# Performance work log

Measured on AMD Instinct MI355X. Metric: run time of the kernel, lower is better.

## Reference

```python
import jax, jax.numpy as jnp
import numpy as np

C = 512
NH = 8
GROUPS = 32
EPS = 1e-5


def setup_inputs() -> dict:
    key = jax.random.key(0)
    ks = jax.random.split(key, 7)
    B, T, H, W = 4, 24, 32, 32
    x = jax.random.normal(ks[0], (B, C, T, H, W), dtype=jnp.float32)
    gn_w = jnp.ones((C,), jnp.float32)
    gn_b = jnp.zeros((C,), jnp.float32)
    # 1x1 Conv1d weights stored as [out_ch, in_ch] (kernel dim of size 1 dropped)
    qkv_w = jax.random.normal(ks[1], (3 * C, C), dtype=jnp.float32) / np.sqrt(C)
    qkv_b = jax.random.normal(ks[2], (3 * C,), dtype=jnp.float32) * 0.02
    proj_w = jax.random.normal(ks[3], (C, C), dtype=jnp.float32) / np.sqrt(C)
    proj_b = jax.random.normal(ks[4], (C,), dtype=jnp.float32) * 0.02
    return {"x": x, "gn_w": gn_w, "gn_b": gn_b, "qkv_w": qkv_w,
            "qkv_b": qkv_b, "proj_w": proj_w, "proj_b": proj_b}


def reference(x, gn_w, gn_b, qkv_w, qkv_b, proj_w, proj_b):
    B, Cc, T, H, W = x.shape
    hd = Cc // NH
    # [B,C,T,H,W] -> [B*H*W, C, T]
    xf = jnp.transpose(x, (0, 3, 4, 1, 2)).reshape(B * H * W, Cc, T)
    # GroupNorm over (C/G, T) per group
    xg = xf.reshape(-1, GROUPS, Cc // GROUPS, T)
    mean = xg.mean(axis=(2, 3), keepdims=True)
    var = xg.var(axis=(2, 3), keepdims=True)
    xn = ((xg - mean) * jax.lax.rsqrt(var + EPS)).reshape(-1, Cc, T)
    xn = xn * gn_w[:, None] + gn_b[:, None]
    # 1x1 conv QKV: [n, 3C, T]
    qkv = jnp.einsum('nct,dc->ndt', xn, qkv_w) + qkv_b[:, None]
    qkv = qkv.reshape(-1, 3, NH, hd, T)
    q, k, v = qkv[:, 0], qkv[:, 1], qkv[:, 2]  # each [n, h, d, T]
    scale = 1.0 / np.sqrt(hd)
    attn = jax.nn.softmax(jnp.einsum('nhdt,nhds->nhts', q, k) * scale, axis=-1)
    out = jnp.einsum('nhts,nhds->nhtd', attn, v)        # [n, h, T, d]
    out = out.transpose(0, 2, 1, 3).reshape(-1, T, Cc)   # [n, T, C]
    out = out.transpose(0, 2, 1)                         # [n, C, T]
    out = jnp.einsum('nct,dc->ndt', out, proj_w) + proj_b[:, None]
    out = out.reshape(B, H, W, Cc, T).transpose(0, 3, 4, 1, 2)
    return x + out
```

## Files before the change

kernel.cpp:

```cpp
#include <hip/hip_runtime.h>
#include <hip/hip_bf16.h>
#include <stdint.h>

#define C_    512
#define T_    24
#define HWSZ  1024
#define NN    4096
#define JTOT  98304
#define EPSV  1e-5f

typedef short short8 __attribute__((ext_vector_type(8)));
typedef short short4v __attribute__((ext_vector_type(4)));
typedef float f32x4 __attribute__((ext_vector_type(4)));
typedef float f32x2 __attribute__((ext_vector_type(2)));
typedef __bf16 bf16x2 __attribute__((ext_vector_type(2)));

typedef __attribute__((address_space(1))) const uint32_t glob_u32;
typedef __attribute__((address_space(3))) uint32_t lds_u32;

#if __has_builtin(__builtin_amdgcn_fdot2_f32_bf16)
#define HAS_DOT2 1
#else
#define HAS_DOT2 0
#endif

__device__ __forceinline__ unsigned short f2bf(float f) {
  union { float f; unsigned u; } v; v.f = f;
  unsigned r = v.u + 0x7fffu + ((v.u >> 16) & 1u);
  return (unsigned short)(r >> 16);
}
__device__ __forceinline__ float bf2f(unsigned short b) {
  union { unsigned u; float f; } v; v.u = ((unsigned)b) << 16;
  return v.f;
}
__device__ __forceinline__ float bflo(uint32_t u) {
  union { unsigned u; float f; } v; v.u = u << 16; return v.f;
}
__device__ __forceinline__ float bfhi(uint32_t u) {
  union { unsigned u; float f; } v; v.u = u & 0xffff0000u; return v.f;
}
__device__ __forceinline__ uint32_t pkbf(float a, float b) {
  return (uint32_t)f2bf(a) | ((uint32_t)f2bf(b) << 16);
}
__device__ __forceinline__ bf16x2 asbf2(uint32_t u) {
  union { uint32_t u; bf16x2 v; } c; c.u = u; return c.v;
}

__device__ __forceinline__ void gload_lds16(const void* g, void* l) {
  __builtin_amdgcn_global_load_lds((glob_u32*)g, (lds_u32*)l, 16, 0, 0);
}

__global__ void k_cvt(const float* __restrict__ qkvw, const float* __restrict__ projw,
                      unsigned short* __restrict__ qkvw_bf, unsigned short* __restrict__ projw_bf) {
  int i = blockIdx.x * 256 + threadIdx.x;
  if (i < 786432) qkvw_bf[i] = f2bf(qkvw[i]);
  if (i < 262144) projw_bf[i] = f2bf(projw[i]);
}

__global__ __launch_bounds__(256) void k_stats(const float* __restrict__ x,
                                               float* __restrict__ mean, float* __restrict__ rstd) {
  int bid = blockIdx.x;
  int g = bid & 31, hwt = (bid >> 5) & 15, b = bid >> 9;
  int tid = threadIdx.x, lane = tid & 63, grp = tid >> 6;
  int hw = hwt * 64 + lane;
  float s = 0.f, sq = 0.f;
  for (int ct = grp; ct < 384; ct += 4) {
    int c = g * 16 + ct / 24;
    int t = ct % 24;
    float v = x[((size_t)((b * 512 + c) * 24 + t) << 10) + hw];
    s += v; sq += v * v;
  }
  __shared__ float ls[4][64], lq[4][64];
  ls[grp][lane] = s; lq[grp][lane] = sq;
  __syncthreads();
  if (tid < 64) {
    float S = ls[0][tid] + ls[1][tid] + ls[2][tid] + ls[3][tid];
    float Q = lq[0][tid] + lq[1][tid] + lq[2][tid] + lq[3][tid];
    float m = S * (1.f / 384.f);
    float var = Q * (1.f / 384.f) - m * m;
    int n = b * HWSZ + hwt * 64 + tid;
    mean[n * 32 + g] = m;
    rstd[n * 32 + g] = rsqrtf(var + EPSV);
  }
}

__global__ __launch_bounds__(256) void k_norm(const float* __restrict__ x,
                                              const float* __restrict__ mean, const float* __restrict__ rstd,
                                              const float* __restrict__ gnw, const float* __restrict__ gnb,
                                              unsigned short* __restrict__ xn) {
  __shared__ unsigned short xs[64][260];
  const int bid = blockIdx.x;
  const int hwt = bid & 15;
  const int chalf = (bid >> 4) & 1;
  const int tb = bid >> 5;
  const int t = tb % 24, b = tb / 24;
  const int hw0 = hwt * 64;
  const int tid = threadIdx.x;
  const int w = tid >> 6, lane = tid & 63;

  const int cslot = w * 4 + (lane >> 4);
  const int hwr = (lane & 15) * 4;
#pragma unroll
  for (int k = 0; k < 8; ++k) {
    const int crel = k * 32 + cslot * 2;
    const int c = chalf * 256 + crel;
    const float4 v0 = *reinterpret_cast<const float4*>(
        &x[(((size_t)(b * 512 + c) * 24 + t) << 10) + hw0 + hwr]);
    const float4 v1 = *reinterpret_cast<const float4*>(
        &x[(((size_t)(b * 512 + c + 1) * 24 + t) << 10) + hw0 + hwr]);
    *reinterpret_cast<uint32_t*>(&xs[hwr + 0][crel]) = pkbf(v0.x, v1.x);
    *reinterpret_cast<uint32_t*>(&xs[hwr + 1][crel]) = pkbf(v0.y, v1.y);
    *reinterpret_cast<uint32_t*>(&xs[hwr + 2][crel]) = pkbf(v0.z, v1.z);
    *reinterpret_cast<uint32_t*>(&xs[hwr + 3][crel]) = pkbf(v0.w, v1.w);
  }

  const int crel8 = (lane & 31) * 8;
  const int c8 = chalf * 256 + crel8;
  const int g = c8 >> 4;
  float gw[8], gb[8];
#pragma unroll
  for (int i = 0; i < 8; ++i) { gw[i] = gnw[c8 + i]; gb[i] = gnb[c8 + i]; }
  float mm[8], rr[8];
#pragma unroll
  for (int p = 0; p < 8; ++p) {
    const int nrel = (p * 4 + w) * 2 + (lane >> 5);
    const int ng = b * HWSZ + hw0 + nrel;
    mm[p] = mean[ng * 32 + g];
    rr[p] = rstd[ng * 32 + g];
  }
  __syncthreads();

#pragma unroll
  for (int p = 0; p < 8; ++p) {
    const int nrel = (p * 4 + w) * 2 + (lane >> 5);
    const short4v lo = *reinterpret_cast<const short4v*>(&xs[nrel][crel8]);
    const short4v hi = *reinterpret_cast<const short4v*>(&xs[nrel][crel8 + 4]);
    float y[8];
#pragma unroll
    for (int i = 0; i < 4; ++i) {
      y[i]     = (bf2f((unsigned short)lo[i]) - mm[p]) * rr[p] * gw[i]     + gb[i];
      y[i + 4] = (bf2f((unsigned short)hi[i]) - mm[p]) * rr[p] * gw[i + 4] + gb[i + 4];
    }
    uint4 wv;
    wv.x = pkbf(y[0], y[1]);
    wv.y = pkbf(y[2], y[3]);
    wv.z = pkbf(y[4], y[5]);
    wv.w = pkbf(y[6], y[7]);
    const size_t j = (size_t)t * NN + b * HWSZ + hw0 + nrel;
    *reinterpret_cast<uint4*>(&xn[j * C_ + c8]) = wv;
  }
}

#define STAGE8(mat, half, tile, Gptr, row0)                                           \
  {                                                                                   \
    unsigned short* _l = &lds[(((tile) & 1) * 2 + (mat))][half][(w * 2) * 512];       \
    const unsigned short* _g = (Gptr) +                                               \
        (size_t)((row0) + (half) * 128 + (w * 2) * 8 + srow) * 512 +                  \
        (tile) * 64 + sslot * 8;                                                      \
    gload_lds16(_g, _l);                                                              \
    gload_lds16(_g + 8 * 512, _l + 512);                                              \
  }

__global__ __launch_bounds__(512, 2) void k_gemm8(
    const unsigned short* __restrict__ A,
    const unsigned short* __restrict__ B,
    const float* __restrict__ bias,
    unsigned short* __restrict__ outb) {
  __shared__ __attribute__((aligned(16))) unsigned short lds[4][2][8192];
  const int bid = blockIdx.x;
  const int cpx = 2304 >> 3;
  const int lid = (bid & 7) * cpx + (bid >> 3);
  const int mt = lid % 6, jt = lid / 6;
  const int m0 = mt * 256, j0 = jt * 256;
  const int tid = threadIdx.x;
  const int w = tid >> 6, lane = tid & 63;
  const int l16 = lane & 15, lqq = lane >> 4;
  const int wm = w >> 2, wn = w & 3;
  const int srow = lane >> 3;
  const int sslot = (lane & 7) ^ srow;
  const int k0off = l16 * 64 + ((lqq ^ (l16 & 7)) * 8);
  const int k1off = l16 * 64 + (((lqq + 4) ^ (l16 & 7)) * 8);

  f32x4 acc[8][4];
#pragma unroll
  for (int i = 0; i < 8; ++i)
#pragma unroll
    for (int j = 0; j < 4; ++j) acc[i][j] = {0.f, 0.f, 0.f, 0.f};

  STAGE8(0, 0, 0, A, m0); STAGE8(0, 1, 0, A, m0);
  STAGE8(1, 0, 0, B, j0); STAGE8(1, 1, 0, B, j0);
  STAGE8(0, 0, 1, A, m0); STAGE8(0, 1, 1, A, m0);
  STAGE8(1, 0, 1, B, j0);
  asm volatile("s_waitcnt vmcnt(6)" ::: "memory");
  __builtin_amdgcn_s_barrier();

  for (int t = 0; t < 8; ++t) {
    const int buf = t & 1;
    const unsigned short* Ab = &lds[buf * 2 + 0][wm][0];
    const unsigned short* Bb = &lds[buf * 2 + 1][wn >> 1][(wn & 1) * 4096];
    short8 a[8][2], bb[4][2];
#pragma unroll
    for (int rr = 0; rr < 8; ++rr) {
      a[rr][0] = *reinterpret_cast<const short8*>(Ab + rr * 1024 + k0off);
      a[rr][1] = *reinterpret_cast<const short8*>(Ab + rr * 1024 + k1off);
    }
#pragma unroll
    for (int cc = 0; cc < 2; ++cc) {
      bb[cc][0] = *reinterpret_cast<const short8*>(Bb + cc * 1024 + k0off);
      bb[cc][1] = *reinterpret_cast<const short8*>(Bb + cc * 1024 + k1off);
    }
    if (t < 7) STAGE8(1, 1, t + 1, B, j0);
    asm volatile("" ::: "memory");
    __builtin_amdgcn_s_barrier();
    asm volatile("s_waitcnt lgkmcnt(0)" ::: "memory");
    __builtin_amdgcn_sched_barrier(0);
    __builtin_amdgcn_s_setprio(1);
#pragma unroll
    for (int rr = 0; rr < 4; ++rr)
#pragma unroll
      for (int cc = 0; cc < 2; ++cc) {
        acc[rr][cc] = __builtin_amdgcn_mfma_f32_16x16x32_bf16(a[rr][0], bb[cc][0], acc[rr][cc], 0, 0, 0);
        acc[rr][cc] = __builtin_amdgcn_mfma_f32_16x16x32_bf16(a[rr][1], bb[cc][1], acc[rr][cc], 0, 0, 0);
      }
    __builtin_amdgcn_s_setprio(0);
    asm volatile("" ::: "memory");
    __builtin_amdgcn_s_barrier();
#pragma unroll
    for (int cc = 2; cc < 4; ++cc) {
      bb[cc][0] = *reinterpret_cast<const short8*>(Bb + cc * 1024 + k0off);
      bb[cc][1] = *reinterpret_cast<const short8*>(Bb + cc * 1024 + k1off);
    }
    if (t < 6) STAGE8(0, 0, t + 2, A, m0);
    asm volatile("" ::: "memory");
    __builtin_amdgcn_s_barrier();
    asm volatile("s_waitcnt lgkmcnt(0)" ::: "memory");
    __builtin_amdgcn_sched_barrier(0);
    __builtin_amdgcn_s_setprio(1);
#pragma unroll
    for (int rr = 0; rr < 4; ++rr)
#pragma unroll
      for (int cc = 2; cc < 4; ++cc) {
        acc[rr][cc] = __builtin_amdgcn_mfma_f32_16x16x32_bf16(a[rr][0], bb[cc][0], acc[rr][cc], 0, 0, 0);
        acc[rr][cc] = __builtin_amdgcn_mfma_f32_16x16x32_bf16(a[rr][1], bb[cc][1], acc[rr][cc], 0, 0, 0);
      }
    __builtin_amdgcn_s_setprio(0);
    asm volatile("" ::: "memory");
    __builtin_amdgcn_s_barrier();
    if (t < 6) STAGE8(0, 1, t + 2, A, m0);
    asm volatile("" ::: "memory");
    __builtin_amdgcn_s_barrier();
    __builtin_amdgcn_s_setprio(1);
#pragma unroll
    for (int rr = 4; rr < 8; ++rr)
#pragma unroll
      for (int cc = 0; cc < 2; ++cc) {
        acc[rr][cc] = __builtin_amdgcn_mfma_f32_16x16x32_bf16(a[rr][0], bb[cc][0], acc[rr][cc], 0, 0, 0);
        acc[rr][cc] = __builtin_amdgcn_mfma_f32_16x16x32_bf16(a[rr][1], bb[cc][1], acc[rr][cc], 0, 0, 0);
      }
    __builtin_amdgcn_s_setprio(0);
    asm volatile("" ::: "memory");
    __builtin_amdgcn_s_barrier();
    if (t < 6) STAGE8(1, 0, t + 2, B, j0);
    asm volatile("" ::: "memory");
    __builtin_amdgcn_s_barrier();
    __builtin_amdgcn_s_setprio(1);
#pragma unroll
    for (int rr = 4; rr < 8; ++rr)
#pragma unroll
      for (int cc = 2; cc < 4; ++cc) {
        acc[rr][cc] = __builtin_amdgcn_mfma_f32_16x16x32_bf16(a[rr][0], bb[cc][0], acc[rr][cc], 0, 0, 0);
        acc[rr][cc] = __builtin_amdgcn_mfma_f32_16x16x32_bf16(a[rr][1], bb[cc][1], acc[rr][cc], 0, 0, 0);
      }
    __builtin_amdgcn_s_setprio(0);
    asm volatile("" ::: "memory");
    if (t < 6) {
      asm volatile("s_waitcnt vmcnt(6)" ::: "memory");
    } else if (t == 6) {
      asm volatile("s_waitcnt vmcnt(0)" ::: "memory");
    }
    __builtin_amdgcn_s_barrier();
  }

#pragma unroll
  for (int rr = 0; rr < 8; ++rr) {
#pragma unroll
    for (int cc = 0; cc < 4; ++cc) {
      const int row = m0 + wm * 128 + rr * 16 + lqq * 4;
      const int col = j0 + wn * 64 + cc * 16 + l16;
#pragma unroll
      for (int r = 0; r < 4; ++r) {
        float v = acc[rr][cc][r] + bias[row + r];
        outb[(size_t)(row + r) * JTOT + col] = f2bf(v);
      }
    }
  }
}

__global__ __launch_bounds__(256, 3) void k_proj(
    const unsigned short* __restrict__ A,
    const unsigned short* __restrict__ B,
    const float* __restrict__ bias,
    const float* __restrict__ xres,
    float* __restrict__ outf) {
  __shared__ __attribute__((aligned(16))) unsigned short As[2][8192];
  const int bid = blockIdx.x;
  const int cpx = 3072 >> 3;
  const int lid = (bid & 7) * cpx + (bid >> 3);
  const int mt = lid & 3, jt = lid >> 2;
  const int m0 = mt * 128, j0 = jt * 128;
  const int tid = threadIdx.x;
  const int w = tid >> 6, lane = tid & 63;
  const int l16 = lane & 15, lqq = lane >> 4;
  const int wm = w >> 1, wn = w & 1;
  const int srow8 = lane >> 3;
  const int sslot = (lane & 7) ^ srow8;
  const int k0off = l16 * 64 + ((lqq ^ (l16 & 7)) * 8);
  const int k1off = l16 * 64 + (((lqq + 4) ^ (l16 & 7)) * 8);

  f32x4 acc[4][4];
#pragma unroll
  for (int i = 0; i < 4; ++i)
#pragma unroll
    for (int j = 0; j < 4; ++j) acc[i][j] = {0.f, 0.f, 0.f, 0.f};

#define PSTAGE(buf, tile)                                                             \
  {                                                                                   \
    _Pragma("unroll")                                                                 \
    for (int m_ = 0; m_ < 4; ++m_) {                                                  \
      unsigned short* _l = &As[buf][m_ * 2048 + w * 512];                             \
      const unsigned short* _g = A +                                                  \
          (size_t)(m0 + m_ * 32 + w * 8 + srow8) * 512 + (tile) * 64 + sslot * 8;     \
      gload_lds16(_g, _l);                                                            \
    }                                                                                 \
  }

#define LOADB(dst, tt)                                                                \
  {                                                                                   \
    _Pragma("unroll")                                                                 \
    for (int cc = 0; cc < 4; ++cc) {                                                  \
      const int jj_ = j0 + wn * 64 + cc * 16 + l16;                                   \
      _Pragma("unroll")                                                               \
      for (int ks = 0; ks < 2; ++ks)                                                  \
        dst[cc][ks] = *reinterpret_cast<const short8*>(                               \
            &B[((size_t)((tt) * 8 + ks * 4 + lqq) * JTOT + jj_) * 8]);                \
    }                                                                                 \
  }

#define PSTEP(t, CUR, NXT)                                                            \
  {                                                                                   \
    if ((t) < 7) { PSTAGE(((t) + 1) & 1, (t) + 1); LOADB(NXT, (t) + 1); }             \
    const unsigned short* Ab = &As[(t) & 1][(wm * 64) * 64];                          \
    _Pragma("unroll")                                                                 \
    for (int rr = 0; rr < 4; ++rr) {                                                  \
      short8 a0 = *reinterpret_cast<const short8*>(Ab + rr * 1024 + k0off);           \
      short8 a1 = *reinterpret_cast<const short8*>(Ab + rr * 1024 + k1off);           \
      _Pragma("unroll")                                                               \
      for (int cc = 0; cc < 4; ++cc) {                                                \
        acc[rr][cc] = __builtin_amdgcn_mfma_f32_16x16x32_bf16(a0, CUR[cc][0], acc[rr][cc], 0, 0, 0); \
        acc[rr][cc] = __builtin_amdgcn_mfma_f32_16x16x32_bf16(a1, CUR[cc][1], acc[rr][cc], 0, 0, 0); \
      }                                                                               \
    }                                                                                 \
    __syncthreads();                                                                  \
  }

  short8 bbA[4][2], bbB[4][2];
  PSTAGE(0, 0);
  LOADB(bbA, 0);
  __syncthreads();

  PSTEP(0, bbA, bbB);
  PSTEP(1, bbB, bbA);
  PSTEP(2, bbA, bbB);
  PSTEP(3, bbB, bbA);
  PSTEP(4, bbA, bbB);
  PSTEP(5, bbB, bbA);
  PSTEP(6, bbA, bbB);
  PSTEP(7, bbB, bbA);

#pragma unroll
  for (int mi = 0; mi < 4; ++mi) {
#pragma unroll
    for (int ni = 0; ni < 4; ++ni) {
      const int dbase = m0 + wm * 64 + mi * 16 + lqq * 4;
      const int jj = j0 + wn * 64 + ni * 16 + l16;
      const int t_ = jj >> 12, n = jj & 4095;
      const int b_ = n >> 10, hw = n & 1023;
#pragma unroll
      for (int r = 0; r < 4; ++r) {
        size_t o = (((size_t)(b_ * 512 + dbase + r) * 24 + t_) << 10) + hw;
        outf[o] = xres[o] + acc[mi][ni][r] + bias[dbase + r];
      }
    }
  }
}

__global__ __launch_bounds__(512) void k_attn(const unsigned short* __restrict__ qkv,
                                              unsigned short* __restrict__ aoC) {
  __shared__ uint32_t kq[2][4][24][64];
  const int ntile = blockIdx.x, h = blockIdx.y;
  const int n0 = ntile * 64;
  const int tid = threadIdx.x;
  const int lane = tid & 63, slot = tid >> 6;
  const int t0 = slot * 3;
  const size_t bq = (size_t)(h * 64) * JTOT;
  const size_t bk = (size_t)(512 + h * 64) * JTOT;
  const size_t bv = (size_t)(1024 + h * 64) * JTOT;

#define STG_UNIT(matbase, dpv, ttv, segv, dst)                                        \
  {                                                                                   \
    const size_t gb = (matbase) + (size_t)(dc + 2 * (dpv)) * JTOT + (ttv) * NN +      \
                      n0 + (segv) * 8;                                                \
    const uint4 va = *reinterpret_cast<const uint4*>(&qkv[gb]);                       \
    const uint4 vb = *reinterpret_cast<const uint4*>(&qkv[gb + JTOT]);                \
    uint4 w0, w1;                                                                     \
    w0.x = (va.x & 0xffffu) | (vb.x << 16);                                           \
    w0.y = (va.x >> 16) | (vb.x & 0xffff0000u);                                       \
    w0.z = (va.y & 0xffffu) | (vb.y << 16);                                           \
    w0.w = (va.y >> 16) | (vb.y & 0xffff0000u);                                       \
    w1.x = (va.z & 0xffffu) | (vb.z << 16);                                           \
    w1.y = (va.z >> 16) | (vb.z & 0xffff0000u);                                       \
    w1.z = (va.w & 0xffffu) | (vb.w << 16);                                           \
    w1.w = (va.w >> 16) | (vb.w & 0xffff0000u);                                       \
    uint32_t* d_ = &(dst)[dpv][ttv][(segv) * 8];                                      \
    *reinterpret_cast<uint4*>(d_) = w0;                                               \
    *reinterpret_cast<uint4*>(d_ + 4) = w1;                                           \
  }

#define STAGE_QK(c_)                                                                  \
  {                                                                                   \
    const int dc = (c_) * 8;                                                          \
    _Pragma("unroll")                                                                 \
    for (int p = 0; p < 3; ++p) {                                                     \
      const int row = p * 64 + (tid >> 3);                                            \
      const int seg = tid & 7;                                                        \
      if (row < 96) {                                                                 \
        const int dp = row / 24, tt = row % 24;                                       \
        STG_UNIT(bk, dp, tt, seg, kq[0]);                                             \
      } else {                                                                        \
        const int r2 = row - 96;                                                      \
        const int dp = r2 / 24, tt = r2 % 24;                                         \
        STG_UNIT(bq, dp, tt, seg, kq[1]);                                             \
      }                                                                               \
    }                                                                                 \
  }

#define STAGE_V(c_)                                                                   \
  {                                                                                   \
    const int dc = (c_) * 8;                                                          \
    _Pragma("unroll")                                                                 \
    for (int p = 0; p < 2; ++p) {                                                     \
      const int u = p * 512 + tid;                                                    \
      if (u < 768) {                                                                  \
        const int row = u >> 3, seg = u & 7;                                          \
        const int dp = row / 24, tt = row % 24;                                       \
        STG_UNIT(bv, dp, tt, seg, kq[0]);                                             \
      }                                                                               \
    }                                                                                 \
  }

  float S[3][24];
#pragma unroll
  for (int a = 0; a < 3; ++a)
#pragma unroll
    for (int s = 0; s < 24; ++s) S[a][s] = 0.f;

  STAGE_QK(0);
  __syncthreads();
  for (int c = 0; c < 8; ++c) {
    uint32_t qw[3][4];
#pragma unroll
    for (int dp = 0; dp < 4; ++dp)
#pragma unroll
      for (int a = 0; a < 3; ++a)
        qw[a][dp] = kq[1][dp][t0 + a][lane];
#if !HAS_DOT2
    float qf[3][8];
#pragma unroll
    for (int dp = 0; dp < 4; ++dp)
#pragma unroll
      for (int a = 0; a < 3; ++a) {
        qf[a][2 * dp]     = bflo(qw[a][dp]);
        qf[a][2 * dp + 1] = bfhi(qw[a][dp]);
      }
#endif
#pragma unroll
    for (int dp = 0; dp < 4; ++dp) {
#pragma unroll
      for (int s = 0; s < 24; ++s) {
        const uint32_t kpr = kq[0][dp][s][lane];
#if HAS_DOT2
        const bf16x2 k2 = asbf2(kpr);
        S[0][s] = __builtin_amdgcn_fdot2_f32_bf16(asbf2(qw[0][dp]), k2, S[0][s], false);
        S[1][s] = __builtin_amdgcn_fdot2_f32_bf16(asbf2(qw[1][dp]), k2, S[1][s], false);
        S[2][s] = __builtin_amdgcn_fdot2_f32_bf16(asbf2(qw[2][dp]), k2, S[2][s], false);
#else
        const float k0 = bflo(kpr), k1 = bfhi(kpr);
        S[0][s] = fmaf(qf[0][2 * dp], k0, S[0][s]);
        S[0][s] = fmaf(qf[0][2 * dp + 1], k1, S[0][s]);
        S[1][s] = fmaf(qf[1][2 * dp], k0, S[1][s]);
        S[1][s] = fmaf(qf[1][2 * dp + 1], k1, S[1][s]);
        S[2][s] = fmaf(qf[2][2 * dp], k0, S[2][s]);
        S[2][s] = fmaf(qf[2][2 * dp + 1], k1, S[2][s]);
#endif
      }
    }
    __syncthreads();
    if (c < 7) {
      STAGE_QK(c + 1);
      __syncthreads();
    }
  }

#pragma unroll
  for (int a = 0; a < 3; ++a) {
    float mx = S[a][0];
#pragma unroll
    for (int s = 1; s < 24; ++s) mx = fmaxf(mx, S[a][s]);
    float sum = 0.f;
#pragma unroll
    for (int s = 0; s < 24; ++s) {
      float e = __expf((S[a][s] - mx) * 0.125f);
      S[a][s] = e; sum += e;
    }
    float inv = 1.f / sum;
#pragma unroll
    for (int s = 0; s < 24; ++s) S[a][s] *= inv;
  }

  STAGE_V(0);
  __syncthreads();
  for (int c = 0; c < 8; ++c) {
    f32x2 o2[3][4];
#pragma unroll
    for (int a = 0; a < 3; ++a)
#pragma unroll
      for (int dp = 0; dp < 4; ++dp) o2[a][dp] = {0.f, 0.f};
#pragma unroll
    for (int dp = 0; dp < 4; ++dp) {
#pragma unroll
      for (int s = 0; s < 24; ++s) {
        const uint32_t vpr = kq[0][dp][s][lane];
        f32x2 v2;
        v2.x = bflo(vpr);
        v2.y = bfhi(vpr);
        o2[0][dp] += S[0][s] * v2;
        o2[1][dp] += S[1][s] * v2;
        o2[2][dp] += S[2][s] * v2;
      }
    }
#pragma unroll
    for (int a = 0; a < 3; ++a) {
      uint4 wv;
      wv.x = pkbf(o2[a][0].x, o2[a][0].y);
      wv.y = pkbf(o2[a][1].x, o2[a][1].y);
      wv.z = pkbf(o2[a][2].x, o2[a][2].y);
      wv.w = pkbf(o2[a][3].x, o2[a][3].y);
      const size_t unit = (size_t)(h * 8 + c) * JTOT + (size_t)(t0 + slot * 0 + a) * NN + n0 + lane;
      *reinterpret_cast<uint4*>(&aoC[unit * 8]) = wv;
    }
    __syncthreads();
    if (c < 7) {
      STAGE_V(c + 1);
      __syncthreads();
    }
  }
}

extern "C" void kernel_launch(void* const* d_in, const int* in_sizes, int n_in,
                              void* d_out, int out_size, void* d_ws, size_t ws_size,
                              hipStream_t stream) {
  (void)in_sizes; (void)n_in; (void)out_size; (void)ws_size;
  const float* x     = (const float*)d_in[0];
  const float* gnw   = (const float*)d_in[1];
  const float* gnb   = (const float*)d_in[2];
  const float* qkvw  = (const float*)d_in[3];
  const float* qkvb  = (const float*)d_in[4];
  const float* projw = (const float*)d_in[5];
  const float* projb = (const float*)d_in[6];
  float* out = (float*)d_out;
  char* ws = (char*)d_ws;

  unsigned short* qkvw_bf = (unsigned short*)(ws);
  unsigned short* projw_bf = (unsigned short*)(ws + 1572864);
  float* mean = (float*)(ws + 2097152);
  float* rstd = (float*)(ws + 2621440);
  unsigned short* xn  = (unsigned short*)(ws + 3145728);
  unsigned short* qkv = (unsigned short*)(ws + 3145728 + 100663296);

  k_cvt<<<dim3(3072), dim3(256), 0, stream>>>(qkvw, projw, qkvw_bf, projw_bf);
  k_stats<<<dim3(2048), dim3(256), 0, stream>>>(x, mean, rstd);
  k_norm<<<dim3(3072), dim3(256), 0, stream>>>(x, mean, rstd, gnw, gnb, xn);
  k_gemm8<<<dim3(2304), dim3(512), 0, stream>>>(qkvw_bf, xn, qkvb, qkv);
  k_attn<<<dim3(64, 8), dim3(512), 0, stream>>>(qkv, xn);
  k_proj<<<dim3(3072), dim3(256), 0, stream>>>(projw_bf, xn, projb, x, out);
}
```

Baseline: 565.0 us.

## Write QKV in packed pair layout so attention stages via direct LDS loads

The QKV GEMM epilogue now writes pairs of adjacent head-dim channels packed as bf16x2 words, in a blocked layout indexed by matrix, head, channel chunk, dim pair and time. The attention kernel can then stage K, Q and V tiles with global-to-LDS 16-byte loads instead of loading two rows and interleaving them in registers. This removes the repacking ALU work and the register round trip in attention. In exchange the GEMM epilogue does 32-bit stores scattered across blocks, and the attention kernel now depends on a layout contract with the GEMM.

Measured after the change: 533.0 us. 1.06x faster.

```diff
diff --git a/kernel.cpp b/kernel.cpp
--- a/kernel.cpp
+++ b/kernel.cpp
@@ -165,7 +165,7 @@
     const unsigned short* __restrict__ A,
     const unsigned short* __restrict__ B,
     const float* __restrict__ bias,
-    unsigned short* __restrict__ outb) {
+    uint32_t* __restrict__ outP) {
   __shared__ __attribute__((aligned(16))) unsigned short lds[4][2][8192];
   const int bid = blockIdx.x;
   const int cpx = 2304 >> 3;
@@ -287,11 +287,19 @@
     for (int cc = 0; cc < 4; ++cc) {
       const int row = m0 + wm * 128 + rr * 16 + lqq * 4;
       const int col = j0 + wn * 64 + cc * 16 + l16;
-#pragma unroll
-      for (int r = 0; r < 4; ++r) {
-        float v = acc[rr][cc][r] + bias[row + r];
-        outb[(size_t)(row + r) * JTOT + col] = f2bf(v);
-      }
+      const int t_ = col >> 12, n = col & 4095;
+      const int mat = row >> 9;
+      const int hh = (row >> 6) & 7;
+      const int d = row & 63;
+      const int ch = d >> 3;
+      const int dp = (d & 7) >> 1;
+      const size_t blk = (size_t)((((mat * 8 + hh) * 8 + ch) * 4 + dp) * 24 + t_);
+      const float v0 = acc[rr][cc][0] + bias[row];
+      const float v1 = acc[rr][cc][1] + bias[row + 1];
+      const float v2 = acc[rr][cc][2] + bias[row + 2];
+      const float v3 = acc[rr][cc][3] + bias[row + 3];
+      outP[blk * 4096 + n] = pkbf(v0, v1);
+      outP[(blk + 24) * 4096 + n] = pkbf(v2, v3);
     }
   }
 }
@@ -394,7 +402,7 @@
   }
 }
 
-__global__ __launch_bounds__(512) void k_attn(const unsigned short* __restrict__ qkv,
+__global__ __launch_bounds__(512) void k_attn(const uint32_t* __restrict__ qkvP,
                                               unsigned short* __restrict__ aoC) {
   __shared__ uint32_t kq[2][4][24][64];
   const int ntile = blockIdx.x, h = blockIdx.y;
@@ -402,59 +410,39 @@
   const int tid = threadIdx.x;
   const int lane = tid & 63, slot = tid >> 6;
   const int t0 = slot * 3;
-  const size_t bq = (size_t)(h * 64) * JTOT;
-  const size_t bk = (size_t)(512 + h * 64) * JTOT;
-  const size_t bv = (size_t)(1024 + h * 64) * JTOT;
-
-#define STG_UNIT(matbase, dpv, ttv, segv, dst)                                        \
-  {                                                                                   \
-    const size_t gb = (matbase) + (size_t)(dc + 2 * (dpv)) * JTOT + (ttv) * NN +      \
-                      n0 + (segv) * 8;                                                \
-    const uint4 va = *reinterpret_cast<const uint4*>(&qkv[gb]);                       \
-    const uint4 vb = *reinterpret_cast<const uint4*>(&qkv[gb + JTOT]);                \
-    uint4 w0, w1;                                                                     \
-    w0.x = (va.x & 0xffffu) | (vb.x << 16);                                           \
-    w0.y = (va.x >> 16) | (vb.x & 0xffff0000u);                                       \
-    w0.z = (va.y & 0xffffu) | (vb.y << 16);                                           \
-    w0.w = (va.y >> 16) | (vb.y & 0xffff0000u);                                       \
-    w1.x = (va.z & 0xffffu) | (vb.z << 16);                                           \
-    w1.y = (va.z >> 16) | (vb.z & 0xffff0000u);                                       \
-    w1.z = (va.w & 0xffffu) | (vb.w << 16);                                           \
-    w1.w = (va.w >> 16) | (vb.w & 0xffff0000u);                                       \
-    uint32_t* d_ = &(dst)[dpv][ttv][(segv) * 8];                                      \
-    *reinterpret_cast<uint4*>(d_) = w0;                                               \
-    *reinterpret_cast<uint4*>(d_ + 4) = w1;                                           \
-  }
+  uint32_t* kqf = &kq[0][0][0][0];
+  const int BLK = 4 * 24 * 4096;
+  const size_t bQ = (size_t)((0 * 8 + h) * 8) * BLK;
+  const size_t bK = (size_t)((1 * 8 + h) * 8) * BLK;
+  const size_t bV = (size_t)((2 * 8 + h) * 8) * BLK;
+  const int ub = tid & 448;
 
 #define STAGE_QK(c_)                                                                  \
   {                                                                                   \
-    const int dc = (c_) * 8;                                                          \
+    const size_t cbk = bK + (size_t)(c_) * BLK;                                       \
+    const size_t cbq = bQ + (size_t)(c_) * BLK;                                       \
     _Pragma("unroll")                                                                 \
     for (int p = 0; p < 3; ++p) {                                                     \
-      const int row = p * 64 + (tid >> 3);                                            \
-      const int seg = tid & 7;                                                        \
-      if (row < 96) {                                                                 \
-        const int dp = row / 24, tt = row % 24;                                       \
-        STG_UNIT(bk, dp, tt, seg, kq[0]);                                             \
-      } else {                                                                        \
-        const int r2 = row - 96;                                                      \
-        const int dp = r2 / 24, tt = r2 % 24;                                         \
-        STG_UNIT(bq, dp, tt, seg, kq[1]);                                             \
-      }                                                                               \
+      const int u = p * 512 + tid;                                                    \
+      gload_lds16(qkvP + cbk + (u >> 4) * 4096 + n0 + (u & 15) * 4,                   \
+                  kqf + (size_t)(p * 512 + ub) * 4);                                  \
+    }                                                                                 \
+    _Pragma("unroll")                                                                 \
+    for (int p = 0; p < 3; ++p) {                                                     \
+      const int u = p * 512 + tid;                                                    \
+      gload_lds16(qkvP + cbq + (u >> 4) * 4096 + n0 + (u & 15) * 4,                   \
+                  kqf + (size_t)(1536 + p * 512 + ub) * 4);                           \
     }                                                                                 \
   }
 
 #define STAGE_V(c_)                                                                   \
   {                                                                                   \
-    const int dc = (c_) * 8;                                                          \
+    const size_t cbv = bV + (size_t)(c_) * BLK;                                       \
     _Pragma("unroll")                                                                 \
-    for (int p = 0; p < 2; ++p) {                                                     \
+    for (int p = 0; p < 3; ++p) {                                                     \
       const int u = p * 512 + tid;                                                    \
-      if (u < 768) {                                                                  \
-        const int row = u >> 3, seg = u & 7;                                          \
-        const int dp = row / 24, tt = row % 24;                                       \
-        STG_UNIT(bv, dp, tt, seg, kq[0]);                                             \
-      }                                                                               \
+      gload_lds16(qkvP + cbv + (u >> 4) * 4096 + n0 + (u & 15) * 4,                   \
+                  kqf + (size_t)(p * 512 + ub) * 4);                                  \
     }                                                                                 \
   }
 
@@ -555,7 +543,7 @@
       wv.y = pkbf(o2[a][1].x, o2[a][1].y);
       wv.z = pkbf(o2[a][2].x, o2[a][2].y);
       wv.w = pkbf(o2[a][3].x, o2[a][3].y);
-      const size_t unit = (size_t)(h * 8 + c) * JTOT + (size_t)(t0 + slot * 0 + a) * NN + n0 + lane;
+      const size_t unit = (size_t)(h * 8 + c) * JTOT + (size_t)(t0 + a) * NN + n0 + lane;
       *reinterpret_cast<uint4*>(&aoC[unit * 8]) = wv;
     }
     __syncthreads();
@@ -585,12 +573,12 @@
   float* mean = (float*)(ws + 2097152);
   float* rstd = (float*)(ws + 2621440);
   unsigned short* xn  = (unsigned short*)(ws + 3145728);
-  unsigned short* qkv = (unsigned short*)(ws + 3145728 + 100663296);
+  uint32_t* qkvP = (uint32_t*)(ws + 3145728 + 100663296);
 
   k_cvt<<<dim3(3072), dim3(256), 0, stream>>>(qkvw, projw, qkvw_bf, projw_bf);
   k_stats<<<dim3(2048), dim3(256), 0, stream>>>(x, mean, rstd);
   k_norm<<<dim3(3072), dim3(256), 0, stream>>>(x, mean, rstd, gnw, gnb, xn);
-  k_gemm8<<<dim3(2304), dim3(512), 0, stream>>>(qkvw_bf, xn, qkvb, qkv);
-  k_attn<<<dim3(64, 8), dim3(512), 0, stream>>>(qkv, xn);
+  k_gemm8<<<dim3(2304), dim3(512), 0, stream>>>(qkvw_bf, xn, qkvb, qkvP);
+  k_attn<<<dim3(64, 8), dim3(512), 0, stream>>>(qkvP, xn);
   k_proj<<<dim3(3072), dim3(256), 0, stream>>>(projw_bf, xn, projb, x, out);
 }
```
